# Optimization experiments

Measured on AMD Instinct MI355X. Metric: run time of the kernel, lower is better.

Reference implementation:

```python
import jax, jax.numpy as jnp
import numpy as np

DIM = 2048
N_EXPERTS = 16
TOP_K = 4
MOE_INTER = 1024
SHARED_INTER = 2 * MOE_INTER  # n_shared_experts * moe_inter_dim
B, S = 4, 1024
INIT = 0.02


def setup_inputs() -> dict:
    key = jax.random.key(0)
    ks = jax.random.split(key, 8)
    return {
        "x": jax.random.normal(ks[0], (B, S, DIM), dtype=jnp.float32),
        "gate_w": jax.random.normal(ks[1], (DIM, N_EXPERTS), dtype=jnp.float32) * INIT,
        "w1": jax.random.normal(ks[2], (N_EXPERTS, DIM, MOE_INTER), dtype=jnp.float32) * INIT,
        "w2": jax.random.normal(ks[3], (N_EXPERTS, MOE_INTER, DIM), dtype=jnp.float32) * INIT,
        "w3": jax.random.normal(ks[4], (N_EXPERTS, DIM, MOE_INTER), dtype=jnp.float32) * INIT,
        "ws1": jax.random.normal(ks[5], (DIM, SHARED_INTER), dtype=jnp.float32) * INIT,
        "ws2": jax.random.normal(ks[6], (SHARED_INTER, DIM), dtype=jnp.float32) * INIT,
        "ws3": jax.random.normal(ks[7], (DIM, SHARED_INTER), dtype=jnp.float32) * INIT,
    }


def _moe_forward(x, gate_w, w1, w2, w3, ws1, ws2, ws3):
    shape = x.shape
    xf = x.reshape(-1, DIM)  # [T, D]
    # Gate: softmax scores, top-k selection (weights are the top-k probs)
    scores = jax.nn.softmax(xf @ gate_w, axis=-1)          # [T, E]
    weights, indices = jax.lax.top_k(scores, TOP_K)         # [T, K] each
    y = jnp.zeros_like(xf)
    # Fixed loop over experts (structural, not over data dims).
    for e in range(N_EXPERTS):
        # gate coefficient for expert e: 0 if not in token's top-k
        coef = jnp.sum(weights * (indices == e), axis=-1)   # [T]
        h = jax.nn.silu(xf @ w1[e]) * (xf @ w3[e])          # [T, I]
        y = y + coef[:, None] * (h @ w2[e])
    # Shared experts (always-on gated MLP)
    z = (jax.nn.silu(xf @ ws1) * (xf @ ws3)) @ ws2
    return (y + z).reshape(shape)


def reference(x, gate_w, w1, w2, w3, ws1, ws2, ws3):
    return _moe_forward(x, gate_w, w1, w2, w3, ws1, ws2, ws3)
```

## Files before the change

### kernel.cpp

```cpp
#include <hip/hip_runtime.h>
#include <hip/hip_bf16.h>
#include <stdint.h>

#define T_TOK 4096
#define DIMD  2048
#define NEXP  16
#define TOPK  4
#define NI    1024
#define NSH   2048

typedef __attribute__((ext_vector_type(8))) short short8;
typedef __attribute__((ext_vector_type(4))) float f32x4;
typedef __attribute__((ext_vector_type(4))) unsigned short u16x4;

__device__ __forceinline__ unsigned short f2bf(float f) {
    union { float f; unsigned u; } v; v.f = f;
    return (unsigned short)((v.u + 0x7fffu + ((v.u >> 16) & 1u)) >> 16);
}

__device__ __forceinline__ void gload16(const void* g, void* l) {
    __builtin_amdgcn_global_load_lds(
        (const __attribute__((address_space(1))) void*)g,
        (__attribute__((address_space(3))) void*)l, 16, 0, 0);
}

__global__ __launch_bounds__(256) void gwt_kernel(const float* __restrict__ gw,
                                                  float* __restrict__ gwT) {
    int i = blockIdx.x * 256 + threadIdx.x;
    int d = i >> 4, e = i & 15;
    gwT[e * DIMD + d] = gw[i];
}

__global__ __launch_bounds__(256) void gate_kernel(const float* __restrict__ x,
                                                   const float* __restrict__ gwT,
                                                   int* __restrict__ blk_cnt,
                                                   int* __restrict__ tk_er,
                                                   float* __restrict__ tk_wv) {
    __shared__ int h[16];
    const int blk = blockIdx.x;
    const int t = blk * 4 + (threadIdx.x >> 6);
    const int lane = threadIdx.x & 63;
    if (threadIdx.x < 16) h[threadIdx.x] = 0;
    __syncthreads();

    const f32x4* xr = (const f32x4*)(x + (size_t)t * DIMD);
    f32x4 xv[8];
#pragma unroll
    for (int i = 0; i < 8; ++i) xv[i] = xr[i * 64 + lane];

    float acc[NEXP];
#pragma unroll
    for (int e = 0; e < NEXP; ++e) {
        const f32x4* gr = (const f32x4*)(gwT + e * DIMD);
        float s = 0.f;
#pragma unroll
        for (int i = 0; i < 8; ++i) {
            f32x4 gv = gr[i * 64 + lane];
            s += xv[i][0] * gv[0] + xv[i][1] * gv[1] +
                 xv[i][2] * gv[2] + xv[i][3] * gv[3];
        }
        acc[e] = s;
    }
#pragma unroll
    for (int e = 0; e < NEXP; ++e) {
        float v = acc[e];
#pragma unroll
        for (int off = 32; off; off >>= 1) v += __shfl_xor(v, off, 64);
        acc[e] = v;
    }
    float m = acc[0];
#pragma unroll
    for (int e = 1; e < NEXP; ++e) m = fmaxf(m, acc[e]);
    float s = 0.f;
#pragma unroll
    for (int e = 0; e < NEXP; ++e) { acc[e] = expf(acc[e] - m); s += acc[e]; }
    float inv = 1.f / s;
#pragma unroll
    for (int e = 0; e < NEXP; ++e) acc[e] *= inv;

    float w4[TOPK]; int i4[TOPK];
#pragma unroll
    for (int k = 0; k < TOPK; ++k) {
        float bv = -1.f; int be = 0;
#pragma unroll
        for (int e = 0; e < NEXP; ++e)
            if (acc[e] > bv) { bv = acc[e]; be = e; }
        w4[k] = bv; i4[k] = be;
#pragma unroll
        for (int e = 0; e < NEXP; ++e)
            if (e == be) acc[e] = -1.f;
    }

    if (lane == 0) {
        int r4[TOPK];
#pragma unroll
        for (int k = 0; k < TOPK; ++k) r4[k] = atomicAdd(&h[i4[k]], 1);
#pragma unroll
        for (int k = 0; k < TOPK; ++k) {
            tk_er[t * 4 + k] = (i4[k] << 20) | r4[k];
            tk_wv[t * 4 + k] = w4[k];
        }
    }
    __syncthreads();
    if (threadIdx.x < 16) blk_cnt[blk * 16 + threadIdx.x] = h[threadIdx.x];
}

__global__ __launch_bounds__(256) void scan_kernel(const int* __restrict__ blk_cnt,
                                                   int* __restrict__ blk_off,
                                                   int* __restrict__ cnt,
                                                   int* __restrict__ offs,
                                                   int* __restrict__ table) {
    __shared__ int gsum[16][17];
    __shared__ int gbase[16][17];
    __shared__ int csh[16];
    int tid = threadIdx.x;
    int e = tid >> 4, g = tid & 15;
    {
        int s = 0;
        for (int b = g * 64; b < g * 64 + 64; ++b) s += blk_cnt[b * 16 + e];
        gsum[e][g] = s;
    }
    __syncthreads();
    if (tid < 16) {
        int run = 0;
        for (int g2 = 0; g2 < 16; ++g2) { gbase[tid][g2] = run; run += gsum[tid][g2]; }
        csh[tid] = run;
        cnt[tid] = run;
    }
    __syncthreads();
    {
        int run = gbase[e][g];
        for (int b = g * 64; b < g * 64 + 64; ++b) {
            blk_off[b * 16 + e] = run;
            run += blk_cnt[b * 16 + e];
        }
    }
    if (tid == 0) {
        int o = 0;
        for (int e2 = 0; e2 < 16; ++e2) { offs[e2] = o; o += csh[e2]; }
        offs[NEXP] = o;
        int ns = 0;
        for (int e2 = 0; e2 < 16; ++e2)
            for (int rb = 0; rb < csh[e2]; rb += 128) {
                table[ns] = (e2 << 16) | rb; ++ns;
            }
        table[255] = ns;
    }
}

__global__ __launch_bounds__(256) void fill_kernel(const int* __restrict__ tk_er,
                                                   const float* __restrict__ tk_wv,
                                                   const int* __restrict__ blk_off,
                                                   int* __restrict__ list,
                                                   float* __restrict__ cw) {
    int i = blockIdx.x * 256 + threadIdx.x;
    int rec = tk_er[i];
    int e = rec >> 20, r = rec & 0xFFFFF;
    int t = i >> 2;
    int ro = blk_off[(t >> 2) * 16 + e] + r;
    list[e * T_TOK + ro] = t;
    cw[e * T_TOK + ro] = tk_wv[i];
}

__global__ __launch_bounds__(256) void cvt_kernel(const float* __restrict__ x,
                                                  unsigned short* __restrict__ xb) {
    int i = blockIdx.x * 256 + threadIdx.x;
    const f32x4* src = (const f32x4*)x;
    f32x4 a = src[i * 2 + 0];
    f32x4 b = src[i * 2 + 1];
    short8 o;
#pragma unroll
    for (int j = 0; j < 4; ++j) o[j] = (short)f2bf(a[j]);
#pragma unroll
    for (int j = 0; j < 4; ++j) o[4 + j] = (short)f2bf(b[j]);
    ((short8*)xb)[i] = o;
}

template <int MODE>
__global__ __launch_bounds__(256) void tq_kernel(const float* __restrict__ src,
                                                 unsigned short* __restrict__ dst,
                                                 int K, int N, size_t dstStrideE) {
    int e = blockIdx.z;
    src += (size_t)e * K * N;
    dst += (size_t)e * dstStrideE;
    __shared__ unsigned short tile[32][36];
    int t = threadIdx.x;
    int k0 = blockIdx.y * 32, n0 = blockIdx.x * 32;
    {
        int row = t >> 3, c4 = (t & 7) * 4;
        f32x4 v = *(const f32x4*)(src + (size_t)(k0 + row) * N + n0 + c4);
#pragma unroll
        for (int j = 0; j < 4; ++j) tile[row][c4 + j] = f2bf(v[j]);
    }
    __syncthreads();
    {
        int nn = t >> 3, kc = (t & 7) * 4;
        int n = n0 + nn;
        int r = (MODE == 0) ? n : ((n >> 4) * 32 + (MODE == 2 ? 16 : 0) + (n & 15));
        u16x4 o;
#pragma unroll
        for (int j = 0; j < 4; ++j) o[j] = tile[kc + j][nn];
        *(u16x4*)(dst + (size_t)r * K + k0 + kc) = o;
    }
}

template <int KIND>
__global__ __launch_bounds__(512, 4) void gemm8p(
    const unsigned short* __restrict__ A, const unsigned short* __restrict__ Ball,
    const int* __restrict__ cnt, const int* __restrict__ offs,
    const int* __restrict__ list, const float* __restrict__ cw,
    unsigned short* __restrict__ hout, float* __restrict__ fout,
    const int* __restrict__ table) {
    constexpr bool ROUTED = (KIND == 1 || KIND == 3);
    constexpr bool UP = (KIND <= 1);
    constexpr int K = (KIND <= 1) ? 2048 : 1024;
    constexpr int NT = K / 32;
    constexpr int ASTR = (KIND == 3) ? 1024 : 2048;
    constexpr int BSTR = (KIND == 3) ? 1024 : 2048;

    int bx, rb, e, M, obase;
    if constexpr (ROUTED) {
        int bid = blockIdx.x;
        int slot = bid >> 3;
        if (slot >= table[255]) return;
        bx = bid & 7;
        int pk = table[slot];
        e = pk >> 16;
        rb = pk & 0xFFFF;
        M = cnt[e];
        obase = offs[e];
    } else {
        bx = blockIdx.x; rb = blockIdx.y * 128; e = 0; M = T_TOK; obase = 0;
    }
    const int kb = (KIND == 2) ? blockIdx.z * 1024 : 0;
    const unsigned short* Bp = Ball +
        (KIND == 1 ? (size_t)e * 2048 * 2048 : KIND == 3 ? (size_t)e * 2048 * 1024 : 0);

    extern __shared__ char smem[];

    const int tid = threadIdx.x;
    const int lane = tid & 63, wid = tid >> 6;
    const int wm = wid >> 2, wn = wid & 3;
    const int fr = lane & 15, fq = lane >> 4;
    const int offR = ((fr >> 1) << 7) + (((((fr & 1) << 2) | fq) ^ (fr >> 1)) << 4);
    const int d16 = tid * 16;

    const unsigned short* pA;
    const unsigned short* pB0;
    const unsigned short* pB1;
    {
        int c = tid, s = c >> 3, sl = (c & 7) ^ (s & 7);
        int rA = 2 * s + (sl >> 2), kk = (sl & 3) * 8;
        int gr = rb + rA;
        int cr = (gr < M) ? gr : (M - 1);
        size_t arow;
        if (KIND == 1)      arow = (size_t)list[e * T_TOK + cr];
        else if (KIND == 3) arow = (size_t)(obase + cr);
        else                arow = (size_t)gr;
        pA = A + arow * ASTR + kb + kk;
    }
#pragma unroll
    for (int u = 0; u < 2; ++u) {
        int c = u * 512 + tid, s = c >> 3, sl = (c & 7) ^ (s & 7);
        int rB = 2 * s + (sl >> 2), kk = (sl & 3) * 8;
        const unsigned short* p = Bp + (size_t)(bx * 256 + rB) * BSTR + kb + kk;
        if (u == 0) pB0 = p; else pB1 = p;
    }

    f32x4 acc[4][4];
#pragma unroll
    for (int m = 0; m < 4; ++m)
#pragma unroll
        for (int n = 0; n < 4; ++n) acc[m][n] = (f32x4)0.f;

    gload16(pA,      (void*)(smem + 0 + d16));
    gload16(pA + 32, (void*)(smem + 8192 + d16));
    gload16(pB0,      (void*)(smem + 24576 + d16));
    gload16(pB1,      (void*)(smem + 24576 + 8192 + d16));
    gload16(pB0 + 32, (void*)(smem + 24576 + 16384 + d16));
    gload16(pB1 + 32, (void*)(smem + 24576 + 16384 + 8192 + d16));
    pA += 64; pB0 += 64; pB1 += 64;
    asm volatile("s_waitcnt vmcnt(0)" ::: "memory");
    __builtin_amdgcn_s_barrier();

    int bA = 0, bA2 = 16384;
    int bB = 0, bB2 = 32768;
    for (int t = 0; t < NT; ++t) {
        short8 aF[4], bF[4];
#pragma unroll
        for (int m = 0; m < 4; ++m)
            aF[m] = *(const short8*)(smem + bA + wm * 4096 + m * 1024 + offR);
#pragma unroll
        for (int n = 0; n < 4; ++n)
            bF[n] = *(const short8*)(smem + 24576 + bB + wn * 4096 + n * 1024 + offR);
        const bool more = (t + 2 < NT);
        if (more) {
            gload16(pA, (void*)(smem + bA2 + d16));
            gload16(pB0, (void*)(smem + 24576 + bB2 + d16));
            gload16(pB1, (void*)(smem + 24576 + bB2 + 8192 + d16));
            pA += 32; pB0 += 32; pB1 += 32;
        }
        __builtin_amdgcn_s_setprio(1);
#pragma unroll
        for (int m = 0; m < 4; ++m)
#pragma unroll
            for (int n = 0; n < 4; ++n)
                acc[m][n] = __builtin_amdgcn_mfma_f32_16x16x32_bf16(aF[m], bF[n], acc[m][n], 0, 0, 0);
        __builtin_amdgcn_s_setprio(0);
        if (more) { asm volatile("s_waitcnt vmcnt(3)" ::: "memory"); }
        else      { asm volatile("s_waitcnt vmcnt(0)" ::: "memory"); }
        __builtin_amdgcn_s_barrier();
        bA = (bA == 16384) ? 0 : bA + 8192;
        bA2 = (bA2 == 16384) ? 0 : bA2 + 8192;
        bB = (bB == 32768) ? 0 : bB + 16384;
        bB2 = (bB2 == 32768) ? 0 : bB2 + 16384;
    }

    if constexpr (UP) {
        constexpr int LDO = (KIND == 1) ? NI : NSH;
#pragma unroll
        for (int m = 0; m < 4; ++m)
#pragma unroll
            for (int q = 0; q < 4; ++q) {
                int gr = rb + wm * 64 + m * 16 + fq * 4 + q;
                if (gr < M) {
                    float coef = 1.f;
                    if constexpr (KIND == 1) coef = cw[e * T_TOK + gr];
                    size_t orow = (size_t)(obase + gr) * LDO;
#pragma unroll
                    for (int nfp = 0; nfp < 2; ++nfp) {
                        float c1 = acc[m][2 * nfp][q], c3 = acc[m][2 * nfp + 1][q];
                        float h = c1 / (1.f + __expf(-c1)) * c3 * coef;
                        int ncol = (bx * 8 + wn * 2 + nfp) * 16 + fr;
                        hout[orow + ncol] = f2bf(h);
                    }
                }
            }
    } else {
#pragma unroll
        for (int m = 0; m < 4; ++m)
#pragma unroll
            for (int q = 0; q < 4; ++q) {
                int gr = rb + wm * 64 + m * 16 + fq * 4 + q;
                if (gr < M) {
                    int orow = (KIND == 3) ? list[e * T_TOK + gr] : gr;
#pragma unroll
                    for (int nf = 0; nf < 4; ++nf) {
                        int col = bx * 256 + wn * 64 + nf * 16 + fr;
                        atomicAdd(fout + (size_t)orow * DIMD + col, acc[m][nf][q]);
                    }
                }
            }
    }
}

extern "C" void kernel_launch(void* const* d_in, const int* in_sizes, int n_in,
                              void* d_out, int out_size, void* d_ws, size_t ws_size,
                              hipStream_t stream) {
    const float* x   = (const float*)d_in[0];
    const float* gw  = (const float*)d_in[1];
    const float* w1  = (const float*)d_in[2];
    const float* w2  = (const float*)d_in[3];
    const float* w3  = (const float*)d_in[4];
    const float* ws1 = (const float*)d_in[5];
    const float* ws2 = (const float*)d_in[6];
    const float* ws3 = (const float*)d_in[7];
    float* out = (float*)d_out;

    char* p = (char*)d_ws;
    unsigned short* xb   = (unsigned short*)p; p += (size_t)T_TOK * DIMD * 2;
    unsigned short* hs   = (unsigned short*)p; p += (size_t)T_TOK * NSH * 2;
    unsigned short* hbuf = (unsigned short*)p; p += (size_t)T_TOK * TOPK * NI * 2;
    unsigned short* upT  = (unsigned short*)p; p += (size_t)NEXP * 2048 * DIMD * 2;
    unsigned short* w2T  = (unsigned short*)p; p += (size_t)NEXP * DIMD * NI * 2;
    unsigned short* upsT = (unsigned short*)p; p += (size_t)2 * NSH * DIMD * 2;
    unsigned short* ws2T = (unsigned short*)p; p += (size_t)DIMD * NSH * 2;
    float* gwT = (float*)p;                    p += (size_t)NEXP * DIMD * 4;
    float* cw = (float*)p;                     p += (size_t)NEXP * T_TOK * 4;
    int* list = (int*)p;                       p += (size_t)NEXP * T_TOK * 4;
    int* tk_er = (int*)p;                      p += (size_t)T_TOK * TOPK * 4;
    float* tk_wv = (float*)p;                  p += (size_t)T_TOK * TOPK * 4;
    int* blk_cnt = (int*)p;                    p += (size_t)1024 * 16 * 4;
    int* blk_off = (int*)p;                    p += (size_t)1024 * 16 * 4;
    int* cnt = (int*)p;                        p += 256;
    int* offs = (int*)p;                       p += 256;
    int* table = (int*)p;                      p += 1024;
    if ((size_t)(p - (char*)d_ws) > ws_size) return;

    hipFuncSetAttribute((const void*)&gemm8p<0>, hipFuncAttributeMaxDynamicSharedMemorySize, 73728);
    hipFuncSetAttribute((const void*)&gemm8p<1>, hipFuncAttributeMaxDynamicSharedMemorySize, 73728);
    hipFuncSetAttribute((const void*)&gemm8p<2>, hipFuncAttributeMaxDynamicSharedMemorySize, 73728);
    hipFuncSetAttribute((const void*)&gemm8p<3>, hipFuncAttributeMaxDynamicSharedMemorySize, 73728);

    hipMemsetAsync(out, 0, (size_t)out_size * 4, stream);
    gwt_kernel<<<(NEXP * DIMD) / 256, 256, 0, stream>>>(gw, gwT);
    gate_kernel<<<T_TOK / 4, 256, 0, stream>>>(x, gwT, blk_cnt, tk_er, tk_wv);
    scan_kernel<<<1, 256, 0, stream>>>(blk_cnt, blk_off, cnt, offs, table);
    fill_kernel<<<T_TOK * TOPK / 256, 256, 0, stream>>>(tk_er, tk_wv, blk_off, list, cw);
    cvt_kernel<<<(T_TOK * DIMD / 8) / 256, 256, 0, stream>>>(x, xb);

    tq_kernel<1><<<dim3(NI / 32, DIMD / 32, NEXP), 256, 0, stream>>>(w1, upT, DIMD, NI, (size_t)2048 * DIMD);
    tq_kernel<2><<<dim3(NI / 32, DIMD / 32, NEXP), 256, 0, stream>>>(w3, upT, DIMD, NI, (size_t)2048 * DIMD);
    tq_kernel<1><<<dim3(NSH / 32, DIMD / 32, 1), 256, 0, stream>>>(ws1, upsT, DIMD, NSH, 0);
    tq_kernel<2><<<dim3(NSH / 32, DIMD / 32, 1), 256, 0, stream>>>(ws3, upsT, DIMD, NSH, 0);
    tq_kernel<0><<<dim3(DIMD / 32, NI / 32, NEXP), 256, 0, stream>>>(w2, w2T, NI, DIMD, (size_t)DIMD * NI);
    tq_kernel<0><<<dim3(DIMD / 32, NSH / 32, 1), 256, 0, stream>>>(ws2, ws2T, NSH, DIMD, 0);

    gemm8p<0><<<dim3(16, 32, 1), 512, 73728, stream>>>(
        xb, upsT, nullptr, nullptr, nullptr, nullptr, hs, nullptr, nullptr);
    gemm8p<2><<<dim3(8, 32, 2), 512, 73728, stream>>>(
        hs, ws2T, nullptr, nullptr, nullptr, nullptr, nullptr, out, nullptr);
    gemm8p<1><<<1152, 512, 73728, stream>>>(
        xb, upT, cnt, offs, list, cw, hbuf, nullptr, table);
    gemm8p<3><<<1152, 512, 73728, stream>>>(
        hbuf, w2T, cnt, offs, list, nullptr, nullptr, out, table);
}
```

Baseline: 708.0 us.

## Use 4 waves per block with 128x64 per-wave tiles in grouped GEMM

The GEMM block drops from 8 waves (2x4 wave grid, 64x64 per wave) to 4 waves that each cover all 128 rows and a 64-column slice. Each wave now reads 8 A fragments and 4 B fragments per k-step, so it issues more MFMAs per LDS read and fewer waves share the barrier. Each thread issues twice as many async global-to-LDS loads, and the waitcnt values are adjusted to match. The cost is doubled accumulator registers per wave (128 fp32) and half the threads per block, which lowers latency hiding and may cause register pressure or spilling.

Measured after the change: 718.9 us. No clear change (+1.5%).

```diff
diff --git a/kernel.cpp b/kernel.cpp
--- a/kernel.cpp
+++ b/kernel.cpp
@@ -205,7 +205,7 @@
 }
 
 template <int KIND>
-__global__ __launch_bounds__(512, 4) void gemm8p(
+__global__ __launch_bounds__(256, 2) void gemm8p(
     const unsigned short* __restrict__ A, const unsigned short* __restrict__ Ball,
     const int* __restrict__ cnt, const int* __restrict__ offs,
     const int* __restrict__ list, const float* __restrict__ cw,
@@ -239,17 +239,17 @@
     extern __shared__ char smem[];
 
     const int tid = threadIdx.x;
-    const int lane = tid & 63, wid = tid >> 6;
-    const int wm = wid >> 2, wn = wid & 3;
+    const int lane = tid & 63;
+    const int wn = tid >> 6;
     const int fr = lane & 15, fq = lane >> 4;
     const int offR = ((fr >> 1) << 7) + (((((fr & 1) << 2) | fq) ^ (fr >> 1)) << 4);
     const int d16 = tid * 16;
 
-    const unsigned short* pA;
-    const unsigned short* pB0;
-    const unsigned short* pB1;
-    {
-        int c = tid, s = c >> 3, sl = (c & 7) ^ (s & 7);
+    const unsigned short* pA[2];
+    const unsigned short* pB[4];
+#pragma unroll
+    for (int i = 0; i < 2; ++i) {
+        int c = i * 256 + tid, s = c >> 3, sl = (c & 7) ^ (s & 7);
         int rA = 2 * s + (sl >> 2), kk = (sl & 3) * 8;
         int gr = rb + rA;
         int cr = (gr < M) ? gr : (M - 1);
@@ -257,57 +257,65 @@
         if (KIND == 1)      arow = (size_t)list[e * T_TOK + cr];
         else if (KIND == 3) arow = (size_t)(obase + cr);
         else                arow = (size_t)gr;
-        pA = A + arow * ASTR + kb + kk;
-    }
-#pragma unroll
-    for (int u = 0; u < 2; ++u) {
-        int c = u * 512 + tid, s = c >> 3, sl = (c & 7) ^ (s & 7);
+        pA[i] = A + arow * ASTR + kb + kk;
+    }
+#pragma unroll
+    for (int i = 0; i < 4; ++i) {
+        int c = i * 256 + tid, s = c >> 3, sl = (c & 7) ^ (s & 7);
         int rB = 2 * s + (sl >> 2), kk = (sl & 3) * 8;
-        const unsigned short* p = Bp + (size_t)(bx * 256 + rB) * BSTR + kb + kk;
-        if (u == 0) pB0 = p; else pB1 = p;
-    }
-
-    f32x4 acc[4][4];
-#pragma unroll
-    for (int m = 0; m < 4; ++m)
+        pB[i] = Bp + (size_t)(bx * 256 + rB) * BSTR + kb + kk;
+    }
+
+    f32x4 acc[8][4];
+#pragma unroll
+    for (int m = 0; m < 8; ++m)
 #pragma unroll
         for (int n = 0; n < 4; ++n) acc[m][n] = (f32x4)0.f;
 
-    gload16(pA,      (void*)(smem + 0 + d16));
-    gload16(pA + 32, (void*)(smem + 8192 + d16));
-    gload16(pB0,      (void*)(smem + 24576 + d16));
-    gload16(pB1,      (void*)(smem + 24576 + 8192 + d16));
-    gload16(pB0 + 32, (void*)(smem + 24576 + 16384 + d16));
-    gload16(pB1 + 32, (void*)(smem + 24576 + 16384 + 8192 + d16));
-    pA += 64; pB0 += 64; pB1 += 64;
-    asm volatile("s_waitcnt vmcnt(0)" ::: "memory");
+#pragma unroll
+    for (int i = 0; i < 2; ++i) gload16(pA[i], (void*)(smem + i * 4096 + d16));
+#pragma unroll
+    for (int i = 0; i < 4; ++i) gload16(pB[i], (void*)(smem + 24576 + i * 4096 + d16));
+#pragma unroll
+    for (int i = 0; i < 2; ++i) gload16(pA[i] + 32, (void*)(smem + 8192 + i * 4096 + d16));
+#pragma unroll
+    for (int i = 0; i < 4; ++i) gload16(pB[i] + 32, (void*)(smem + 24576 + 16384 + i * 4096 + d16));
+#pragma unroll
+    for (int i = 0; i < 2; ++i) pA[i] += 64;
+#pragma unroll
+    for (int i = 0; i < 4; ++i) pB[i] += 64;
+    asm volatile("s_waitcnt vmcnt(6)" ::: "memory");
     __builtin_amdgcn_s_barrier();
 
     int bA = 0, bA2 = 16384;
     int bB = 0, bB2 = 32768;
     for (int t = 0; t < NT; ++t) {
-        short8 aF[4], bF[4];
-#pragma unroll
-        for (int m = 0; m < 4; ++m)
-            aF[m] = *(const short8*)(smem + bA + wm * 4096 + m * 1024 + offR);
+        short8 aF[8], bF[4];
+#pragma unroll
+        for (int m = 0; m < 8; ++m)
+            aF[m] = *(const short8*)(smem + bA + m * 1024 + offR);
 #pragma unroll
         for (int n = 0; n < 4; ++n)
             bF[n] = *(const short8*)(smem + 24576 + bB + wn * 4096 + n * 1024 + offR);
         const bool more = (t + 2 < NT);
         if (more) {
-            gload16(pA, (void*)(smem + bA2 + d16));
-            gload16(pB0, (void*)(smem + 24576 + bB2 + d16));
-            gload16(pB1, (void*)(smem + 24576 + bB2 + 8192 + d16));
-            pA += 32; pB0 += 32; pB1 += 32;
+#pragma unroll
+            for (int i = 0; i < 2; ++i) gload16(pA[i], (void*)(smem + bA2 + i * 4096 + d16));
+#pragma unroll
+            for (int i = 0; i < 4; ++i) gload16(pB[i], (void*)(smem + 24576 + bB2 + i * 4096 + d16));
+#pragma unroll
+            for (int i = 0; i < 2; ++i) pA[i] += 32;
+#pragma unroll
+            for (int i = 0; i < 4; ++i) pB[i] += 32;
         }
         __builtin_amdgcn_s_setprio(1);
 #pragma unroll
-        for (int m = 0; m < 4; ++m)
+        for (int m = 0; m < 8; ++m)
 #pragma unroll
             for (int n = 0; n < 4; ++n)
                 acc[m][n] = __builtin_amdgcn_mfma_f32_16x16x32_bf16(aF[m], bF[n], acc[m][n], 0, 0, 0);
         __builtin_amdgcn_s_setprio(0);
-        if (more) { asm volatile("s_waitcnt vmcnt(3)" ::: "memory"); }
+        if (more) { asm volatile("s_waitcnt vmcnt(6)" ::: "memory"); }
         else      { asm volatile("s_waitcnt vmcnt(0)" ::: "memory"); }
         __builtin_amdgcn_s_barrier();
         bA = (bA == 16384) ? 0 : bA + 8192;
@@ -319,10 +327,10 @@
     if constexpr (UP) {
         constexpr int LDO = (KIND == 1) ? NI : NSH;
 #pragma unroll
-        for (int m = 0; m < 4; ++m)
+        for (int m = 0; m < 8; ++m)
 #pragma unroll
             for (int q = 0; q < 4; ++q) {
-                int gr = rb + wm * 64 + m * 16 + fq * 4 + q;
+                int gr = rb + m * 16 + fq * 4 + q;
                 if (gr < M) {
                     float coef = 1.f;
                     if constexpr (KIND == 1) coef = cw[e * T_TOK + gr];
@@ -338,10 +346,10 @@
             }
     } else {
 #pragma unroll
-        for (int m = 0; m < 4; ++m)
+        for (int m = 0; m < 8; ++m)
 #pragma unroll
             for (int q = 0; q < 4; ++q) {
-                int gr = rb + wm * 64 + m * 16 + fq * 4 + q;
+                int gr = rb + m * 16 + fq * 4 + q;
                 if (gr < M) {
                     int orow = (KIND == 3) ? list[e * T_TOK + gr] : gr;
 #pragma unroll
@@ -406,12 +414,12 @@
     tq_kernel<0><<<dim3(DIMD / 32, NI / 32, NEXP), 256, 0, stream>>>(w2, w2T, NI, DIMD, (size_t)DIMD * NI);
     tq_kernel<0><<<dim3(DIMD / 32, NSH / 32, 1), 256, 0, stream>>>(ws2, ws2T, NSH, DIMD, 0);
 
-    gemm8p<0><<<dim3(16, 32, 1), 512, 73728, stream>>>(
+    gemm8p<0><<<dim3(16, 32, 1), 256, 73728, stream>>>(
         xb, upsT, nullptr, nullptr, nullptr, nullptr, hs, nullptr, nullptr);
-    gemm8p<2><<<dim3(8, 32, 2), 512, 73728, stream>>>(
+    gemm8p<2><<<dim3(8, 32, 2), 256, 73728, stream>>>(
         hs, ws2T, nullptr, nullptr, nullptr, nullptr, nullptr, out, nullptr);
-    gemm8p<1><<<1152, 512, 73728, stream>>>(
+    gemm8p<1><<<1152, 256, 73728, stream>>>(
         xb, upT, cnt, offs, list, cw, hbuf, nullptr, table);
-    gemm8p<3><<<1152, 512, 73728, stream>>>(
+    gemm8p<3><<<1152, 256, 73728, stream>>>(
         hbuf, w2T, cnt, offs, list, nullptr, nullptr, out, table);
 }
```

## Fuse shared and routed expert GEMMs into single launches, widen transpose tiles

Applied to the files above, without the earlier changes.

Merges the shared-expert and routed-expert GEMMs into one launch per phase (up and down). Block indices below 512 handle the shared expert and the rest handle routed tiles, which removes launch gaps and lets the two workloads fill the GPU together. The weight transpose/convert kernels now use 64x64 tiles with 8-wide stores, and w1/w3 are handled in a single paired kernel, cutting the number of launches. Launch bounds drop from 4 to 2 waves per SIMD, which may lower occupancy, and the runtime routed/shared branching adds some register pressure.

Result: faster. 663.9 us (-6.2%).

```diff
diff --git a/kernel.cpp b/kernel.cpp
--- a/kernel.cpp
+++ b/kernel.cpp
@@ -12,6 +12,7 @@
 typedef __attribute__((ext_vector_type(8))) short short8;
 typedef __attribute__((ext_vector_type(4))) float f32x4;
 typedef __attribute__((ext_vector_type(4))) unsigned short u16x4;
+typedef __attribute__((ext_vector_type(8))) unsigned short u16x8;
 
 __device__ __forceinline__ unsigned short f2bf(float f) {
     union { float f; unsigned u; } v; v.f = f;
@@ -176,65 +177,109 @@
     ((short8*)xb)[i] = o;
 }
 
-template <int MODE>
-__global__ __launch_bounds__(256) void tq_kernel(const float* __restrict__ src,
-                                                 unsigned short* __restrict__ dst,
-                                                 int K, int N, size_t dstStrideE) {
+__global__ __launch_bounds__(256) void tq_pair(const float* __restrict__ s1,
+                                               const float* __restrict__ s3,
+                                               unsigned short* __restrict__ dst,
+                                               int K, int N,
+                                               size_t srcStrideE, size_t dstStrideE) {
     int e = blockIdx.z;
-    src += (size_t)e * K * N;
+    s1 += (size_t)e * srcStrideE;
+    s3 += (size_t)e * srcStrideE;
     dst += (size_t)e * dstStrideE;
-    __shared__ unsigned short tile[32][36];
-    int t = threadIdx.x;
-    int k0 = blockIdx.y * 32, n0 = blockIdx.x * 32;
-    {
-        int row = t >> 3, c4 = (t & 7) * 4;
-        f32x4 v = *(const f32x4*)(src + (size_t)(k0 + row) * N + n0 + c4);
-#pragma unroll
-        for (int j = 0; j < 4; ++j) tile[row][c4 + j] = f2bf(v[j]);
+    __shared__ unsigned short tile[64][72];
+    const int t = threadIdx.x;
+    const int k0 = blockIdx.y * 64, n0 = blockIdx.x * 64;
+    const int lr = t >> 4, lc4 = (t & 15) * 4;
+    const int sr8 = (t & 7) * 8, sn = t >> 3;
+#pragma unroll
+    for (int half = 0; half < 2; ++half) {
+        const float* src = half ? s3 : s1;
+#pragma unroll
+        for (int r = 0; r < 4; ++r) {
+            f32x4 v = *(const f32x4*)(src + (size_t)(k0 + lr + r * 16) * N + n0 + lc4);
+#pragma unroll
+            for (int j = 0; j < 4; ++j) tile[lr + r * 16][lc4 + j] = f2bf(v[j]);
+        }
+        __syncthreads();
+#pragma unroll
+        for (int q = 0; q < 2; ++q) {
+            int nn = sn + q * 32;
+            int n = n0 + nn;
+            int rrow = (n >> 4) * 32 + half * 16 + (n & 15);
+            u16x8 o;
+#pragma unroll
+            for (int j = 0; j < 8; ++j) o[j] = tile[sr8 + j][nn];
+            *(u16x8*)(dst + (size_t)rrow * K + k0 + sr8) = o;
+        }
+        __syncthreads();
+    }
+}
+
+__global__ __launch_bounds__(256) void tq_plain(const float* __restrict__ src,
+                                                unsigned short* __restrict__ dst,
+                                                int K, int N,
+                                                size_t srcStrideE, size_t dstStrideE) {
+    int e = blockIdx.z;
+    src += (size_t)e * srcStrideE;
+    dst += (size_t)e * dstStrideE;
+    __shared__ unsigned short tile[64][72];
+    const int t = threadIdx.x;
+    const int k0 = blockIdx.y * 64, n0 = blockIdx.x * 64;
+    const int lr = t >> 4, lc4 = (t & 15) * 4;
+    const int sr8 = (t & 7) * 8, sn = t >> 3;
+#pragma unroll
+    for (int r = 0; r < 4; ++r) {
+        f32x4 v = *(const f32x4*)(src + (size_t)(k0 + lr + r * 16) * N + n0 + lc4);
+#pragma unroll
+        for (int j = 0; j < 4; ++j) tile[lr + r * 16][lc4 + j] = f2bf(v[j]);
     }
     __syncthreads();
-    {
-        int nn = t >> 3, kc = (t & 7) * 4;
+#pragma unroll
+    for (int q = 0; q < 2; ++q) {
+        int nn = sn + q * 32;
         int n = n0 + nn;
-        int r = (MODE == 0) ? n : ((n >> 4) * 32 + (MODE == 2 ? 16 : 0) + (n & 15));
-        u16x4 o;
-#pragma unroll
-        for (int j = 0; j < 4; ++j) o[j] = tile[kc + j][nn];
-        *(u16x4*)(dst + (size_t)r * K + k0 + kc) = o;
-    }
-}
-
-template <int KIND>
-__global__ __launch_bounds__(512, 4) void gemm8p(
-    const unsigned short* __restrict__ A, const unsigned short* __restrict__ Ball,
+        u16x8 o;
+#pragma unroll
+        for (int j = 0; j < 8; ++j) o[j] = tile[sr8 + j][nn];
+        *(u16x8*)(dst + (size_t)n * K + k0 + sr8) = o;
+    }
+}
+
+template <bool UP>
+__global__ __launch_bounds__(512, 2) void gemm_f(
+    const unsigned short* __restrict__ Ash, const unsigned short* __restrict__ Art,
+    const unsigned short* __restrict__ Bsh, const unsigned short* __restrict__ Brt,
     const int* __restrict__ cnt, const int* __restrict__ offs,
     const int* __restrict__ list, const float* __restrict__ cw,
-    unsigned short* __restrict__ hout, float* __restrict__ fout,
-    const int* __restrict__ table) {
-    constexpr bool ROUTED = (KIND == 1 || KIND == 3);
-    constexpr bool UP = (KIND <= 1);
-    constexpr int K = (KIND <= 1) ? 2048 : 1024;
-    constexpr int NT = K / 32;
-    constexpr int ASTR = (KIND == 3) ? 1024 : 2048;
-    constexpr int BSTR = (KIND == 3) ? 1024 : 2048;
-
-    int bx, rb, e, M, obase;
-    if constexpr (ROUTED) {
-        int bid = blockIdx.x;
-        int slot = bid >> 3;
+    unsigned short* __restrict__ hs, unsigned short* __restrict__ hbuf,
+    float* __restrict__ fout, const int* __restrict__ table) {
+    constexpr int NT = UP ? 64 : 32;
+
+    const int bid = blockIdx.x;
+    const bool routed = bid >= 512;
+    int bx, rb, e = 0, M, obase = 0, kb = 0;
+    const unsigned short* Ap;
+    const unsigned short* Bp;
+    int ASTRr, BSTRr;
+    if (!routed) {
+        if (UP) { bx = bid & 15; rb = (bid >> 4) * 128; }
+        else    { bx = bid & 7;  rb = ((bid >> 3) & 31) * 128; kb = (bid >> 8) * 1024; }
+        M = T_TOK;
+        Ap = Ash; Bp = Bsh;
+        ASTRr = 2048; BSTRr = 2048;
+    } else {
+        int rbid = bid - 512;
+        int slot = rbid >> 3;
         if (slot >= table[255]) return;
-        bx = bid & 7;
+        bx = rbid & 7;
         int pk = table[slot];
-        e = pk >> 16;
-        rb = pk & 0xFFFF;
-        M = cnt[e];
-        obase = offs[e];
-    } else {
-        bx = blockIdx.x; rb = blockIdx.y * 128; e = 0; M = T_TOK; obase = 0;
-    }
-    const int kb = (KIND == 2) ? blockIdx.z * 1024 : 0;
-    const unsigned short* Bp = Ball +
-        (KIND == 1 ? (size_t)e * 2048 * 2048 : KIND == 3 ? (size_t)e * 2048 * 1024 : 0);
+        e = pk >> 16; rb = pk & 0xFFFF;
+        M = cnt[e]; obase = offs[e];
+        Ap = Art;
+        Bp = Brt + (UP ? (size_t)e * 2048 * 2048 : (size_t)e * 2048 * 1024);
+        ASTRr = UP ? 2048 : 1024;
+        BSTRr = UP ? 2048 : 1024;
+    }
 
     extern __shared__ char smem[];
 
@@ -254,16 +299,16 @@
         int gr = rb + rA;
         int cr = (gr < M) ? gr : (M - 1);
         size_t arow;
-        if (KIND == 1)      arow = (size_t)list[e * T_TOK + cr];
-        else if (KIND == 3) arow = (size_t)(obase + cr);
-        else                arow = (size_t)gr;
-        pA = A + arow * ASTR + kb + kk;
+        if (!routed)  arow = (size_t)gr;
+        else if (UP)  arow = (size_t)list[e * T_TOK + cr];
+        else          arow = (size_t)(obase + cr);
+        pA = Ap + arow * ASTRr + kb + kk;
     }
 #pragma unroll
     for (int u = 0; u < 2; ++u) {
         int c = u * 512 + tid, s = c >> 3, sl = (c & 7) ^ (s & 7);
         int rB = 2 * s + (sl >> 2), kk = (sl & 3) * 8;
-        const unsigned short* p = Bp + (size_t)(bx * 256 + rB) * BSTR + kb + kk;
+        const unsigned short* p = Bp + (size_t)(bx * 256 + rB) * BSTRr + kb + kk;
         if (u == 0) pB0 = p; else pB1 = p;
     }
 
@@ -317,22 +362,22 @@
     }
 
     if constexpr (UP) {
-        constexpr int LDO = (KIND == 1) ? NI : NSH;
+        const int LDO = routed ? NI : NSH;
+        unsigned short* hp = routed ? hbuf : hs;
 #pragma unroll
         for (int m = 0; m < 4; ++m)
 #pragma unroll
             for (int q = 0; q < 4; ++q) {
                 int gr = rb + wm * 64 + m * 16 + fq * 4 + q;
                 if (gr < M) {
-                    float coef = 1.f;
-                    if constexpr (KIND == 1) coef = cw[e * T_TOK + gr];
-                    size_t orow = (size_t)(obase + gr) * LDO;
+                    float coef = routed ? cw[e * T_TOK + gr] : 1.f;
+                    size_t orow = (size_t)((routed ? obase : 0) + gr) * LDO;
 #pragma unroll
                     for (int nfp = 0; nfp < 2; ++nfp) {
                         float c1 = acc[m][2 * nfp][q], c3 = acc[m][2 * nfp + 1][q];
                         float h = c1 / (1.f + __expf(-c1)) * c3 * coef;
                         int ncol = (bx * 8 + wn * 2 + nfp) * 16 + fr;
-                        hout[orow + ncol] = f2bf(h);
+                        hp[orow + ncol] = f2bf(h);
                     }
                 }
             }
@@ -343,7 +388,7 @@
             for (int q = 0; q < 4; ++q) {
                 int gr = rb + wm * 64 + m * 16 + fq * 4 + q;
                 if (gr < M) {
-                    int orow = (KIND == 3) ? list[e * T_TOK + gr] : gr;
+                    int orow = routed ? list[e * T_TOK + gr] : gr;
 #pragma unroll
                     for (int nf = 0; nf < 4; ++nf) {
                         int col = bx * 256 + wn * 64 + nf * 16 + fr;
@@ -387,10 +432,8 @@
     int* table = (int*)p;                      p += 1024;
     if ((size_t)(p - (char*)d_ws) > ws_size) return;
 
-    hipFuncSetAttribute((const void*)&gemm8p<0>, hipFuncAttributeMaxDynamicSharedMemorySize, 73728);
-    hipFuncSetAttribute((const void*)&gemm8p<1>, hipFuncAttributeMaxDynamicSharedMemorySize, 73728);
-    hipFuncSetAttribute((const void*)&gemm8p<2>, hipFuncAttributeMaxDynamicSharedMemorySize, 73728);
-    hipFuncSetAttribute((const void*)&gemm8p<3>, hipFuncAttributeMaxDynamicSharedMemorySize, 73728);
+    hipFuncSetAttribute((const void*)&gemm_f<true>, hipFuncAttributeMaxDynamicSharedMemorySize, 73728);
+    hipFuncSetAttribute((const void*)&gemm_f<false>, hipFuncAttributeMaxDynamicSharedMemorySize, 73728);
 
     hipMemsetAsync(out, 0, (size_t)out_size * 4, stream);
     gwt_kernel<<<(NEXP * DIMD) / 256, 256, 0, stream>>>(gw, gwT);
@@ -399,19 +442,17 @@
     fill_kernel<<<T_TOK * TOPK / 256, 256, 0, stream>>>(tk_er, tk_wv, blk_off, list, cw);
     cvt_kernel<<<(T_TOK * DIMD / 8) / 256, 256, 0, stream>>>(x, xb);
 
-    tq_kernel<1><<<dim3(NI / 32, DIMD / 32, NEXP), 256, 0, stream>>>(w1, upT, DIMD, NI, (size_t)2048 * DIMD);
-    tq_kernel<2><<<dim3(NI / 32, DIMD / 32, NEXP), 256, 0, stream>>>(w3, upT, DIMD, NI, (size_t)2048 * DIMD);
-    tq_kernel<1><<<dim3(NSH / 32, DIMD / 32, 1), 256, 0, stream>>>(ws1, upsT, DIMD, NSH, 0);
-    tq_kernel<2><<<dim3(NSH / 32, DIMD / 32, 1), 256, 0, stream>>>(ws3, upsT, DIMD, NSH, 0);
-    tq_kernel<0><<<dim3(DIMD / 32, NI / 32, NEXP), 256, 0, stream>>>(w2, w2T, NI, DIMD, (size_t)DIMD * NI);
-    tq_kernel<0><<<dim3(DIMD / 32, NSH / 32, 1), 256, 0, stream>>>(ws2, ws2T, NSH, DIMD, 0);
-
-    gemm8p<0><<<dim3(16, 32, 1), 512, 73728, stream>>>(
-        xb, upsT, nullptr, nullptr, nullptr, nullptr, hs, nullptr, nullptr);
-    gemm8p<2><<<dim3(8, 32, 2), 512, 73728, stream>>>(
-        hs, ws2T, nullptr, nullptr, nullptr, nullptr, nullptr, out, nullptr);
-    gemm8p<1><<<1152, 512, 73728, stream>>>(
-        xb, upT, cnt, offs, list, cw, hbuf, nullptr, table);
-    gemm8p<3><<<1152, 512, 73728, stream>>>(
-        hbuf, w2T, cnt, offs, list, nullptr, nullptr, out, table);
-}
+    tq_pair<<<dim3(NI / 64, DIMD / 64, NEXP), 256, 0, stream>>>(
+        w1, w3, upT, DIMD, NI, (size_t)DIMD * NI, (size_t)2048 * DIMD);
+    tq_pair<<<dim3(NSH / 64, DIMD / 64, 1), 256, 0, stream>>>(
+        ws1, ws3, upsT, DIMD, NSH, 0, 0);
+    tq_plain<<<dim3(DIMD / 64, NI / 64, NEXP), 256, 0, stream>>>(
+        w2, w2T, NI, DIMD, (size_t)NI * DIMD, (size_t)DIMD * NI);
+    tq_plain<<<dim3(DIMD / 64, NSH / 64, 1), 256, 0, stream>>>(
+        ws2, ws2T, NSH, DIMD, 0, 0);
+
+    gemm_f<true><<<512 + 144 * 8, 512, 73728, stream>>>(
+        xb, xb, upsT, upT, cnt, offs, list, cw, hs, hbuf, nullptr, table);
+    gemm_f<false><<<512 + 144 * 8, 512, 73728, stream>>>(
+        hs, hbuf, ws2T, w2T, cnt, offs, list, nullptr, nullptr, nullptr, out, table);
+}
```
